# Kernel optimization log

Measured on AMD Instinct MI355X. Metric: run time of the kernel, lower is better.

## Reference

```python
import jax, jax.numpy as jnp
import numpy as np

L, D, H, FF = 4, 512, 8, 1024
B, S = 8, 480
TPT = 15          # TOKENS_PER_TURN
FIELD_IDX = 0
CAP = 6.0         # tanh logit soft cap
NEG = -1e30


def _layer_norm(x, g, b, eps=1e-5):
    m = jnp.mean(x, axis=-1, keepdims=True)
    v = jnp.mean((x - m) ** 2, axis=-1, keepdims=True)
    return (x - m) * jax.lax.rsqrt(v + eps) * g + b


def _episodic_mask(expanded_ids, n_prev_fields):
    # pokemon_batched_episodic_mask, vectorized -> [B, S, S] bool
    idx = jnp.arange(S)
    q_t = (idx // TPT)[:, None]            # [S,1]
    kv_t = (idx // TPT)[None, :]           # [1,S]
    kv_i = (idx % TPT)[None, :]
    same_turn = q_t == kv_t
    prev_field = (kv_i == FIELD_IDX) & (kv_t < q_t) & (q_t - kv_t <= n_prev_fields)
    same_ep = expanded_ids[:, :, None] == expanded_ids[:, None, :]  # [B,S,S]
    return same_ep & (same_turn | prev_field)[None]


def setup_inputs() -> dict:
    key = jax.random.key(0)
    ks = jax.random.split(key, 6)
    x = jax.random.normal(ks[0], (B, S, D), dtype=jnp.float32)
    expanded_ids = jnp.sort(jax.random.randint(ks[1], (B, S), 0, 3), axis=-1)
    inp = {
        "x": x,
        "expanded_ids": expanded_ids,
        "n_prev_fields": 8,
        "Wqkv": 0.02 * jax.random.normal(ks[2], (L, D, 3 * D), dtype=jnp.float32),
        "bqkv": jnp.zeros((L, 3 * D), jnp.float32),
        "Wo": 0.02 * jax.random.normal(ks[3], (L, D, D), dtype=jnp.float32),
        "bo": jnp.zeros((L, D), jnp.float32),
        "g1": jnp.ones((L, D), jnp.float32),
        "b1": jnp.zeros((L, D), jnp.float32),
        "g2": jnp.ones((L, D), jnp.float32),
        "b2": jnp.zeros((L, D), jnp.float32),
        "W1": 0.02 * jax.random.normal(ks[4], (L, D, FF), dtype=jnp.float32),
        "bf1": jnp.zeros((L, FF), jnp.float32),
        "W2": 0.02 * jax.random.normal(ks[5], (L, FF, D), dtype=jnp.float32),
        "bf2": jnp.zeros((L, D), jnp.float32),
    }
    return inp


def _encoder_layer(x, mask, Wqkv, bqkv, Wo, bo, g1, b1, g2, b2, W1, bf1, W2, bf2):
    hd = D // H
    h = _layer_norm(x, g1, b1)
    qkv = h @ Wqkv + bqkv                               # [B,S,3D]
    qkv = qkv.reshape(B, S, 3, H, hd)
    q, k, v = (qkv[:, :, i].transpose(0, 2, 1, 3) for i in range(3))  # [B,H,S,hd]
    scores = jnp.einsum("bhqd,bhkd->bhqk", q, k) / jnp.sqrt(jnp.float32(hd))
    scores = CAP * jnp.tanh(scores / CAP)               # logit soft cap (score_mod)
    scores = jnp.where(mask[:, None], scores, NEG)      # episodic block mask
    attn = jax.nn.softmax(scores, axis=-1)
    out = jnp.einsum("bhqk,bhkd->bhqd", attn, v)
    out = out.transpose(0, 2, 1, 3).reshape(B, S, D)
    x = x + (out @ Wo + bo)
    h2 = _layer_norm(x, g2, b2)
    ff = jax.nn.gelu(h2 @ W1 + bf1, approximate=False) @ W2 + bf2
    return x + ff


def reference(x, expanded_ids, n_prev_fields, Wqkv, bqkv, Wo, bo, g1, b1, g2, b2, W1, bf1, W2, bf2):
    mask = _episodic_mask(expanded_ids, n_prev_fields)
    for l in range(L):
        x = _encoder_layer(x, mask, Wqkv[l], bqkv[l], Wo[l], bo[l],
                           g1[l], b1[l], g2[l], b2[l], W1[l], bf1[l], W2[l], bf2[l])
    return x
```

## Files before the change

kernel.cpp:

```cpp
#include <hip/hip_runtime.h>
#include <hip/hip_bf16.h>
#include <hip/hip_fp16.h>
#include <math.h>

#define NL 4
#define Dm 512
#define FFD 1024
#define Bb 8
#define Ss 480
#define TPT 15
#define ROWS (Bb*Ss)

typedef __attribute__((ext_vector_type(8))) short short8v;
typedef __attribute__((ext_vector_type(4))) float f32x4;
typedef __attribute__((ext_vector_type(2))) _Float16 half2v;
typedef __attribute__((ext_vector_type(8))) _Float16 half8v;

#if __has_builtin(__builtin_amdgcn_fdot2)
#define FDOT2(a, b, c) __builtin_amdgcn_fdot2(a, b, c, false)
#else
#define FDOT2(a, b, c) ((c) + (float)(a)[0] * (float)(b)[0] + (float)(a)[1] * (float)(b)[1])
#endif

__device__ __forceinline__ void gld_lds16(const void* g, void* lbase) {
#if __has_builtin(__builtin_amdgcn_global_load_lds)
    __builtin_amdgcn_global_load_lds((const __attribute__((address_space(1))) void*)g,
                                     (__attribute__((address_space(3))) void*)lbase, 16, 0, 0);
#else
    (void)g; (void)lbase;
#endif
}

__global__ __launch_bounds__(256) void ln_kernel(const float* __restrict__ x,
                                                 const float* __restrict__ g,
                                                 const float* __restrict__ b,
                                                 __hip_bfloat16* __restrict__ out) {
    int w = threadIdx.x >> 6, lane = threadIdx.x & 63;
    int row = blockIdx.x * 4 + w;
    const float* xr = x + (size_t)row * Dm + lane * 8;
    float4 v0 = *(const float4*)xr;
    float4 v1 = *(const float4*)(xr + 4);
    float v[8] = { v0.x, v0.y, v0.z, v0.w, v1.x, v1.y, v1.z, v1.w };

    float s = 0.0f;
#pragma unroll
    for (int e = 0; e < 8; e++) s += v[e];
#pragma unroll
    for (int off = 1; off < 64; off <<= 1) s += __shfl_xor(s, off);
    float mean = s * (1.0f / Dm);

    float ss = 0.0f;
#pragma unroll
    for (int e = 0; e < 8; e++) { v[e] -= mean; ss += v[e] * v[e]; }
#pragma unroll
    for (int off = 1; off < 64; off <<= 1) ss += __shfl_xor(ss, off);
    float rstd = rsqrtf(ss * (1.0f / Dm) + 1e-5f);

    const float* gp = g + lane * 8;
    const float* bp = b + lane * 8;
    float4 g0 = *(const float4*)gp, g1 = *(const float4*)(gp + 4);
    float4 b0 = *(const float4*)bp, b1 = *(const float4*)(bp + 4);
    float gg[8] = { g0.x, g0.y, g0.z, g0.w, g1.x, g1.y, g1.z, g1.w };
    float bb[8] = { b0.x, b0.y, b0.z, b0.w, b1.x, b1.y, b1.z, b1.w };
    short8v pack;
#pragma unroll
    for (int e = 0; e < 8; e++) {
        __hip_bfloat16 t = __float2bfloat16(v[e] * rstd * gg[e] + bb[e]);
        pack[e] = __builtin_bit_cast(short, t);
    }
    *(short8v*)&out[(size_t)row * Dm + lane * 8] = pack;
}

__global__ __launch_bounds__(256) void conv_all(const float* __restrict__ Wqkv,
                                                const float* __restrict__ Wo,
                                                const float* __restrict__ W1,
                                                const float* __restrict__ W2,
                                                __hip_bfloat16* __restrict__ oq,
                                                __hip_bfloat16* __restrict__ oo,
                                                __hip_bfloat16* __restrict__ o1,
                                                __hip_bfloat16* __restrict__ o2) {
    int type = blockIdx.z >> 2, l = blockIdx.z & 3;
    int K, N; const float* src; __hip_bfloat16* dst;
    if (type == 0)      { K = 512;  N = 1536; src = Wqkv; dst = oq; }
    else if (type == 1) { K = 512;  N = 512;  src = Wo;   dst = oo; }
    else if (type == 2) { K = 512;  N = 1024; src = W1;   dst = o1; }
    else                { K = 1024; N = 512;  src = W2;   dst = o2; }
    int n0 = blockIdx.x * 32, k0 = blockIdx.y * 32;
    if (n0 >= N || k0 >= K) return;
    src += (size_t)l * K * N;
    dst += (size_t)l * K * N;

    __shared__ float t[32][33];
    int tx = threadIdx.x & 31, ty = threadIdx.x >> 5;
#pragma unroll
    for (int r = 0; r < 4; r++)
        t[ty * 4 + r][tx] = src[(size_t)(k0 + ty * 4 + r) * N + n0 + tx];
    __syncthreads();
#pragma unroll
    for (int r = 0; r < 4; r++)
        dst[(size_t)(n0 + ty * 4 + r) * K + k0 + tx] = __float2bfloat16(t[tx][ty * 4 + r]);
}

template <int BM, int ACT, int RES, int OUTMODE>
__global__ __launch_bounds__(256) void gemm_mfma(const __hip_bfloat16* __restrict__ A,
                                                 const __hip_bfloat16* __restrict__ Bt,
                                                 const float* __restrict__ bias,
                                                 const float* __restrict__ res,
                                                 void* __restrict__ C,
                                                 int M, int N, int K) {
    constexpr int MF = BM / 32;
    constexpr int ACc = BM / 32;
    __shared__ __align__(16) short As[2][BM * 64];
    __shared__ __align__(16) short Bs[2][64 * 64];

    int lin = blockIdx.y * gridDim.x + blockIdx.x;
    int nwg = gridDim.x * gridDim.y;
    int qq = nwg >> 3;
    int swz = (lin & 7) * qq + (lin >> 3);
    int bx = swz % gridDim.x, by = swz / gridDim.x;

    const int bm = by * BM, bn = bx * 64;
    const int tid = threadIdx.x;
    const int w = tid >> 6, lane = tid & 63;
    const int wm = (w >> 1) * (BM / 2), wn = (w & 1) * 32;
    const int l16 = lane & 15, lq = lane >> 4;
    const short* Ag = (const short*)A;
    const short* Bg = (const short*)Bt;
    const int nt = K >> 6;

    f32x4 acc[MF][2] = {};

    auto stage = [&](int t, int buf) {
        int k0 = t << 6;
#pragma unroll
        for (int c = 0; c < ACc; ++c) {
            int e = c * 256 + tid;
            int row = e >> 3;
            int csrc = (e & 7) ^ (row & 7);
            gld_lds16(Ag + (size_t)(bm + row) * K + k0 + csrc * 8,
                      &As[buf][(c * 256 + w * 64) * 8]);
        }
#pragma unroll
        for (int c = 0; c < 2; ++c) {
            int e = c * 256 + tid;
            int row = e >> 3;
            int csrc = (e & 7) ^ (row & 7);
            gld_lds16(Bg + (size_t)(bn + row) * K + k0 + csrc * 8,
                      &Bs[buf][(c * 256 + w * 64) * 8]);
        }
    };

    stage(0, 0);
    __syncthreads();
    int cur = 0;
    for (int t = 0; t < nt; ++t) {
        if (t + 1 < nt) stage(t + 1, cur ^ 1);
#pragma unroll
        for (int kc = 0; kc < 2; ++kc) {
            short8v af[MF], bf[2];
#pragma unroll
            for (int i = 0; i < MF; i++) {
                int row = wm + i * 16 + l16;
                int ch = (kc * 4 + lq) ^ (row & 7);
                af[i] = *(const short8v*)(&As[cur][row * 64 + ch * 8]);
            }
#pragma unroll
            for (int j = 0; j < 2; j++) {
                int col = wn + j * 16 + l16;
                int ch2 = (kc * 4 + lq) ^ (col & 7);
                bf[j] = *(const short8v*)(&Bs[cur][col * 64 + ch2 * 8]);
            }
#pragma unroll
            for (int i = 0; i < MF; i++)
#pragma unroll
                for (int j = 0; j < 2; j++)
                    acc[i][j] = __builtin_amdgcn_mfma_f32_16x16x32_bf16(
                        af[i], bf[j], acc[i][j], 0, 0, 0);
        }
        __syncthreads();
        cur ^= 1;
    }

#pragma unroll
    for (int i = 0; i < MF; i++) {
#pragma unroll
        for (int j = 0; j < 2; j++) {
#pragma unroll
            for (int r = 0; r < 4; r++) {
                int mrow = bm + wm + i * 16 + lq * 4 + r;
                int ncol = bn + wn + j * 16 + l16;
                float v = acc[i][j][r] + bias[ncol];
                if (ACT == 1) v = 0.5f * v * (1.0f + erff(v * 0.70710678118f));
                if (RES) v += res[(size_t)mrow * N + ncol];
                if (OUTMODE == 0)      ((float*)C)[(size_t)mrow * N + ncol] = v;
                else if (OUTMODE == 1) ((__hip_bfloat16*)C)[(size_t)mrow * N + ncol] = __float2bfloat16(v);
                else                   ((__half*)C)[(size_t)mrow * N + ncol] = __float2half(v);
            }
        }
    }
}

__global__ __launch_bounds__(256) void attn_sparse(const _Float16* __restrict__ qkv,
                                                   const int* __restrict__ ids,
                                                   const int* __restrict__ npf_p,
                                                   __hip_bfloat16* __restrict__ outb) {
    __shared__ _Float16 qs[4][512];
    __shared__ float ps[4][8][24];
    int w = threadIdx.x >> 6, lane = threadIdx.x & 63;
    int bq = blockIdx.x * 4 + w;
    int q = bq % Ss, b = bq / Ss;
    int npf = npf_p[0];
    int qt = q / TPT;
    int qid = ids[bq];

    *(half8v*)&qs[w][lane * 8] = *(const half8v*)&qkv[(size_t)bq * 1536 + lane * 8];
    __syncthreads();

    int h = lane >> 3, cp = lane & 7;

    half2v qreg[32];
#pragma unroll
    for (int i = 0; i < 32; i++) qreg[i] = *(const half2v*)&qs[w][h * 64 + i * 2];

    float s[3];
#pragma unroll
    for (int i = 0; i < 3; i++) {
        int c = cp + i * 8;
        float sv = -INFINITY;
        if (c < 23) {
            bool ok; int k;
            if (c < 15) { k = qt * TPT + c; ok = true; }
            else { int dt = c - 14; int kt = qt - dt; k = kt * TPT; ok = (kt >= 0) && (dt <= npf); }
            if (ok && ids[b * Ss + k] == qid) {
                const half8v* kr = (const half8v*)&qkv[(size_t)(b * Ss + k) * 1536 + 512 + h * 64];
                float dot = 0.0f;
#pragma unroll
                for (int cch = 0; cch < 8; cch++) {
                    half8v kv = kr[cch];
#pragma unroll
                    for (int e = 0; e < 4; e++) {
                        half2v kk = { kv[e * 2], kv[e * 2 + 1] };
                        dot = FDOT2(qreg[cch * 4 + e], kk, dot);
                    }
                }
                float y = dot * (0.125f / 6.0f);
                float e2 = __expf(2.0f * y);
                sv = 6.0f * (e2 - 1.0f) / (e2 + 1.0f);
            }
        }
        s[i] = sv;
    }

    float m = fmaxf(fmaxf(s[0], s[1]), s[2]);
    for (int off = 1; off < 8; off <<= 1) m = fmaxf(m, __shfl_xor(m, off));
    float p0 = __expf(s[0] - m), p1 = __expf(s[1] - m), p2 = __expf(s[2] - m);
    float l = p0 + p1 + p2;
    for (int off = 1; off < 8; off <<= 1) l += __shfl_xor(l, off);
    float inv = 1.0f / l;
    if (cp < 8)       ps[w][h][cp]      = p0 * inv;
    if (cp + 8 < 23)  ps[w][h][cp + 8]  = p1 * inv;
    if (cp + 16 < 23) ps[w][h][cp + 16] = p2 * inv;
    __syncthreads();

    int dg = lane & 7;
    float o[8] = {};
    for (int c = 0; c < 23; c++) {
        float p = ps[w][h][c];
        if (p != 0.0f) {
            int k = (c < 15) ? (qt * TPT + c) : ((qt - (c - 14)) * TPT);
            half8v vv = *(const half8v*)&qkv[(size_t)(b * Ss + k) * 1536 + 1024 + h * 64 + dg * 8];
#pragma unroll
            for (int e = 0; e < 8; e++) o[e] += p * (float)vv[e];
        }
    }
    short8v pack;
#pragma unroll
    for (int e = 0; e < 8; e++) {
        __hip_bfloat16 t = __float2bfloat16(o[e]);
        pack[e] = __builtin_bit_cast(short, t);
    }
    *(short8v*)&outb[(size_t)bq * Dm + h * 64 + dg * 8] = pack;
}

extern "C" void kernel_launch(void* const* d_in, const int* in_sizes, int n_in,
                              void* d_out, int out_size, void* d_ws, size_t ws_size,
                              hipStream_t stream) {
    const float* x    = (const float*)d_in[0];
    const int*   ids  = (const int*)d_in[1];
    const int*   npf  = (const int*)d_in[2];
    const float* Wqkv = (const float*)d_in[3];
    const float* bqkv = (const float*)d_in[4];
    const float* Wo   = (const float*)d_in[5];
    const float* bo   = (const float*)d_in[6];
    const float* g1   = (const float*)d_in[7];
    const float* b1   = (const float*)d_in[8];
    const float* g2   = (const float*)d_in[9];
    const float* b2   = (const float*)d_in[10];
    const float* W1   = (const float*)d_in[11];
    const float* bf1  = (const float*)d_in[12];
    const float* W2   = (const float*)d_in[13];
    const float* bf2  = (const float*)d_in[14];
    float* out = (float*)d_out;

    char* p = (char*)d_ws;
    __hip_bfloat16* hb    = (__hip_bfloat16*)p;   p += (size_t)ROWS * Dm * 2;
    _Float16*       qkvb  = (_Float16*)p;         p += (size_t)ROWS * 3 * Dm * 2;
    __hip_bfloat16* attnb = (__hip_bfloat16*)p;   p += (size_t)ROWS * Dm * 2;
    __hip_bfloat16* fb    = (__hip_bfloat16*)p;   p += (size_t)ROWS * FFD * 2;
    __hip_bfloat16* Wqkv_t= (__hip_bfloat16*)p;   p += (size_t)NL * Dm * 3 * Dm * 2;
    __hip_bfloat16* Wo_t  = (__hip_bfloat16*)p;   p += (size_t)NL * Dm * Dm * 2;
    __hip_bfloat16* W1_t  = (__hip_bfloat16*)p;   p += (size_t)NL * Dm * FFD * 2;
    __hip_bfloat16* W2_t  = (__hip_bfloat16*)p;   p += (size_t)NL * FFD * Dm * 2;

    conv_all<<<dim3(48, 32, 16), 256, 0, stream>>>(Wqkv, Wo, W1, W2,
                                                   Wqkv_t, Wo_t, W1_t, W2_t);

    for (int l = 0; l < NL; l++) {
        const float* xin = (l == 0) ? x : out;
        ln_kernel<<<ROWS / 4, 256, 0, stream>>>(xin, g1 + l * Dm, b1 + l * Dm, hb);
        gemm_mfma<128, 0, 0, 2><<<dim3(24, 30), 256, 0, stream>>>(
            hb, Wqkv_t + (size_t)l * Dm * 3 * Dm, bqkv + l * 3 * Dm, nullptr, qkvb,
            ROWS, 3 * Dm, Dm);
        attn_sparse<<<ROWS / 4, 256, 0, stream>>>(qkvb, ids, npf, attnb);
        gemm_mfma<64, 0, 1, 0><<<dim3(8, 60), 256, 0, stream>>>(
            attnb, Wo_t + (size_t)l * Dm * Dm, bo + l * Dm, xin, out,
            ROWS, Dm, Dm);
        ln_kernel<<<ROWS / 4, 256, 0, stream>>>(out, g2 + l * Dm, b2 + l * Dm, hb);
        gemm_mfma<128, 1, 0, 1><<<dim3(16, 30), 256, 0, stream>>>(
            hb, W1_t + (size_t)l * Dm * FFD, bf1 + l * FFD, nullptr, fb,
            ROWS, FFD, Dm);
        gemm_mfma<64, 0, 1, 0><<<dim3(8, 60), 256, 0, stream>>>(
            fb, W2_t + (size_t)l * FFD * Dm, bf2 + l * Dm, out, out,
            ROWS, Dm, FFD);
    }
}
```

Before: 312.5 us.

## Compact weight-conversion grid, widen N tile for D-output GEMMs, shuffle-based attention probs

The weight-conversion kernel now uses a flat 1D grid with no idle early-exit blocks, replacing the 48x32x16 grid where many blocks did nothing. The GEMM gains a BN template parameter, and the Wo and W2 projections use 64x128 tiles with half as many workgroups. The attention kernel drops its LDS probability buffer and both __syncthreads, broadcasting normalized probabilities via wave shuffles, and swizzles block order. Fewer workgroups for the N=512 GEMMs may underfill the GPU, and the removed barrier relies on each wave reading only its own q slot.

```diff
diff --git a/kernel.cpp b/kernel.cpp
--- a/kernel.cpp
+++ b/kernel.cpp
@@ -79,29 +79,31 @@
                                                 __hip_bfloat16* __restrict__ oo,
                                                 __hip_bfloat16* __restrict__ o1,
                                                 __hip_bfloat16* __restrict__ o2) {
-    int type = blockIdx.z >> 2, l = blockIdx.z & 3;
-    int K, N; const float* src; __hip_bfloat16* dst;
-    if (type == 0)      { K = 512;  N = 1536; src = Wqkv; dst = oq; }
-    else if (type == 1) { K = 512;  N = 512;  src = Wo;   dst = oo; }
-    else if (type == 2) { K = 512;  N = 1024; src = W1;   dst = o1; }
-    else                { K = 1024; N = 512;  src = W2;   dst = o2; }
-    int n0 = blockIdx.x * 32, k0 = blockIdx.y * 32;
-    if (n0 >= N || k0 >= K) return;
+    int bid = blockIdx.x;
+    int l = bid >> 11;
+    int r = bid & 2047;
+    int loc, K, N; const float* src; __hip_bfloat16* dst;
+    if (r < 768)       { loc = r;        K = 512;  N = 1536; src = Wqkv; dst = oq; }
+    else if (r < 1024) { loc = r - 768;  K = 512;  N = 512;  src = Wo;   dst = oo; }
+    else if (r < 1536) { loc = r - 1024; K = 512;  N = 1024; src = W1;   dst = o1; }
+    else               { loc = r - 1536; K = 1024; N = 512;  src = W2;   dst = o2; }
+    int nx = N >> 5;
+    int n0 = (loc % nx) * 32, k0 = (loc / nx) * 32;
     src += (size_t)l * K * N;
     dst += (size_t)l * K * N;
 
     __shared__ float t[32][33];
     int tx = threadIdx.x & 31, ty = threadIdx.x >> 5;
 #pragma unroll
-    for (int r = 0; r < 4; r++)
-        t[ty * 4 + r][tx] = src[(size_t)(k0 + ty * 4 + r) * N + n0 + tx];
+    for (int rr = 0; rr < 4; rr++)
+        t[ty * 4 + rr][tx] = src[(size_t)(k0 + ty * 4 + rr) * N + n0 + tx];
     __syncthreads();
 #pragma unroll
-    for (int r = 0; r < 4; r++)
-        dst[(size_t)(n0 + ty * 4 + r) * K + k0 + tx] = __float2bfloat16(t[tx][ty * 4 + r]);
-}
-
-template <int BM, int ACT, int RES, int OUTMODE>
+    for (int rr = 0; rr < 4; rr++)
+        dst[(size_t)(n0 + ty * 4 + rr) * K + k0 + tx] = __float2bfloat16(t[tx][ty * 4 + rr]);
+}
+
+template <int BM, int BN, int ACT, int RES, int OUTMODE>
 __global__ __launch_bounds__(256) void gemm_mfma(const __hip_bfloat16* __restrict__ A,
                                                  const __hip_bfloat16* __restrict__ Bt,
                                                  const float* __restrict__ bias,
@@ -109,9 +111,11 @@
                                                  void* __restrict__ C,
                                                  int M, int N, int K) {
     constexpr int MF = BM / 32;
+    constexpr int NF = BN / 32;
     constexpr int ACc = BM / 32;
+    constexpr int BCc = BN / 32;
     __shared__ __align__(16) short As[2][BM * 64];
-    __shared__ __align__(16) short Bs[2][64 * 64];
+    __shared__ __align__(16) short Bs[2][BN * 64];
 
     int lin = blockIdx.y * gridDim.x + blockIdx.x;
     int nwg = gridDim.x * gridDim.y;
@@ -119,16 +123,16 @@
     int swz = (lin & 7) * qq + (lin >> 3);
     int bx = swz % gridDim.x, by = swz / gridDim.x;
 
-    const int bm = by * BM, bn = bx * 64;
+    const int bm = by * BM, bn = bx * BN;
     const int tid = threadIdx.x;
     const int w = tid >> 6, lane = tid & 63;
-    const int wm = (w >> 1) * (BM / 2), wn = (w & 1) * 32;
+    const int wm = (w >> 1) * (BM / 2), wn = (w & 1) * (BN / 2);
     const int l16 = lane & 15, lq = lane >> 4;
     const short* Ag = (const short*)A;
     const short* Bg = (const short*)Bt;
     const int nt = K >> 6;
 
-    f32x4 acc[MF][2] = {};
+    f32x4 acc[MF][NF] = {};
 
     auto stage = [&](int t, int buf) {
         int k0 = t << 6;
@@ -141,7 +145,7 @@
                       &As[buf][(c * 256 + w * 64) * 8]);
         }
 #pragma unroll
-        for (int c = 0; c < 2; ++c) {
+        for (int c = 0; c < BCc; ++c) {
             int e = c * 256 + tid;
             int row = e >> 3;
             int csrc = (e & 7) ^ (row & 7);
@@ -157,7 +161,7 @@
         if (t + 1 < nt) stage(t + 1, cur ^ 1);
 #pragma unroll
         for (int kc = 0; kc < 2; ++kc) {
-            short8v af[MF], bf[2];
+            short8v af[MF], bf[NF];
 #pragma unroll
             for (int i = 0; i < MF; i++) {
                 int row = wm + i * 16 + l16;
@@ -165,7 +169,7 @@
                 af[i] = *(const short8v*)(&As[cur][row * 64 + ch * 8]);
             }
 #pragma unroll
-            for (int j = 0; j < 2; j++) {
+            for (int j = 0; j < NF; j++) {
                 int col = wn + j * 16 + l16;
                 int ch2 = (kc * 4 + lq) ^ (col & 7);
                 bf[j] = *(const short8v*)(&Bs[cur][col * 64 + ch2 * 8]);
@@ -173,7 +177,7 @@
 #pragma unroll
             for (int i = 0; i < MF; i++)
 #pragma unroll
-                for (int j = 0; j < 2; j++)
+                for (int j = 0; j < NF; j++)
                     acc[i][j] = __builtin_amdgcn_mfma_f32_16x16x32_bf16(
                         af[i], bf[j], acc[i][j], 0, 0, 0);
         }
@@ -184,7 +188,7 @@
 #pragma unroll
     for (int i = 0; i < MF; i++) {
 #pragma unroll
-        for (int j = 0; j < 2; j++) {
+        for (int j = 0; j < NF; j++) {
 #pragma unroll
             for (int r = 0; r < 4; r++) {
                 int mrow = bm + wm + i * 16 + lq * 4 + r;
@@ -205,16 +209,16 @@
                                                    const int* __restrict__ npf_p,
                                                    __hip_bfloat16* __restrict__ outb) {
     __shared__ _Float16 qs[4][512];
-    __shared__ float ps[4][8][24];
     int w = threadIdx.x >> 6, lane = threadIdx.x & 63;
-    int bq = blockIdx.x * 4 + w;
+    int bid = blockIdx.x;
+    int swb = (bid & 7) * 120 + (bid >> 3);
+    int bq = swb * 4 + w;
     int q = bq % Ss, b = bq / Ss;
     int npf = npf_p[0];
     int qt = q / TPT;
     int qid = ids[bq];
 
     *(half8v*)&qs[w][lane * 8] = *(const half8v*)&qkv[(size_t)bq * 1536 + lane * 8];
-    __syncthreads();
 
     int h = lane >> 3, cp = lane & 7;
 
@@ -257,20 +261,19 @@
     float l = p0 + p1 + p2;
     for (int off = 1; off < 8; off <<= 1) l += __shfl_xor(l, off);
     float inv = 1.0f / l;
-    if (cp < 8)       ps[w][h][cp]      = p0 * inv;
-    if (cp + 8 < 23)  ps[w][h][cp + 8]  = p1 * inv;
-    if (cp + 16 < 23) ps[w][h][cp + 16] = p2 * inv;
-    __syncthreads();
+    float pn0 = p0 * inv, pn1 = p1 * inv, pn2 = p2 * inv;
 
     int dg = lane & 7;
+    int gbase = lane & 56;
     float o[8] = {};
     for (int c = 0; c < 23; c++) {
-        float p = ps[w][h][c];
-        if (p != 0.0f) {
+        float psel = (c < 8) ? pn0 : (c < 16) ? pn1 : pn2;
+        float pj = __shfl(psel, gbase + (c & 7));
+        if (pj > 0.0f) {
             int k = (c < 15) ? (qt * TPT + c) : ((qt - (c - 14)) * TPT);
             half8v vv = *(const half8v*)&qkv[(size_t)(b * Ss + k) * 1536 + 1024 + h * 64 + dg * 8];
 #pragma unroll
-            for (int e = 0; e < 8; e++) o[e] += p * (float)vv[e];
+            for (int e = 0; e < 8; e++) o[e] += pj * (float)vv[e];
         }
     }
     short8v pack;
@@ -312,24 +315,23 @@
     __hip_bfloat16* W1_t  = (__hip_bfloat16*)p;   p += (size_t)NL * Dm * FFD * 2;
     __hip_bfloat16* W2_t  = (__hip_bfloat16*)p;   p += (size_t)NL * FFD * Dm * 2;
 
-    conv_all<<<dim3(48, 32, 16), 256, 0, stream>>>(Wqkv, Wo, W1, W2,
-                                                   Wqkv_t, Wo_t, W1_t, W2_t);
+    conv_all<<<8192, 256, 0, stream>>>(Wqkv, Wo, W1, W2, Wqkv_t, Wo_t, W1_t, W2_t);
 
     for (int l = 0; l < NL; l++) {
         const float* xin = (l == 0) ? x : out;
         ln_kernel<<<ROWS / 4, 256, 0, stream>>>(xin, g1 + l * Dm, b1 + l * Dm, hb);
-        gemm_mfma<128, 0, 0, 2><<<dim3(24, 30), 256, 0, stream>>>(
+        gemm_mfma<128, 64, 0, 0, 2><<<dim3(24, 30), 256, 0, stream>>>(
             hb, Wqkv_t + (size_t)l * Dm * 3 * Dm, bqkv + l * 3 * Dm, nullptr, qkvb,
             ROWS, 3 * Dm, Dm);
         attn_sparse<<<ROWS / 4, 256, 0, stream>>>(qkvb, ids, npf, attnb);
-        gemm_mfma<64, 0, 1, 0><<<dim3(8, 60), 256, 0, stream>>>(
+        gemm_mfma<64, 128, 0, 1, 0><<<dim3(4, 60), 256, 0, stream>>>(
             attnb, Wo_t + (size_t)l * Dm * Dm, bo + l * Dm, xin, out,
             ROWS, Dm, Dm);
         ln_kernel<<<ROWS / 4, 256, 0, stream>>>(out, g2 + l * Dm, b2 + l * Dm, hb);
-        gemm_mfma<128, 1, 0, 1><<<dim3(16, 30), 256, 0, stream>>>(
+        gemm_mfma<128, 64, 1, 0, 1><<<dim3(16, 30), 256, 0, stream>>>(
             hb, W1_t + (size_t)l * Dm * FFD, bf1 + l * FFD, nullptr, fb,
             ROWS, FFD, Dm);
-        gemm_mfma<64, 0, 1, 0><<<dim3(8, 60), 256, 0, stream>>>(
+        gemm_mfma<64, 128, 0, 1, 0><<<dim3(4, 60), 256, 0, stream>>>(
             fb, W2_t + (size_t)l * FFD * Dm, bf2 + l * Dm, out, out,
             ROWS, Dm, FFD);
     }
```

After: 323.8 us. 3.6% more time.
